# Kernel tuning notes

Hardware: AMD Instinct MI355X
Metric: run time of the kernel (lower is better)

Reference implementation:

```python
import jax, jax.numpy as jnp
import numpy as np

N = 50000  # nodes
NEG_SLOPE = 0.2


def gat_conv(x, src, dst, W, a_src, a_dst, b):
    # x: [N, in]; src/dst: [E'] (self-loops already appended)
    h = x @ W                                   # [N, out]
    alpha_s = h @ a_src                         # [N]
    alpha_d = h @ a_dst                         # [N]
    e = alpha_s[src] + alpha_d[dst]             # [E']
    e = jnp.where(e > 0, e, NEG_SLOPE * e)      # leaky_relu
    # segment softmax over destination neighborhoods
    m = jax.ops.segment_max(e, dst, num_segments=N)
    ex = jnp.exp(e - m[dst])
    denom = jax.ops.segment_sum(ex, dst, num_segments=N)
    alpha = ex / denom[dst]                     # [E']
    out = jax.ops.segment_sum(h[src] * alpha[:, None], dst, num_segments=N)
    return out + b


def setup_inputs() -> dict:
    key = jax.random.key(0)
    ks = jax.random.split(key, 16)
    d_in, d_hid, n_cls, E = 256, 256, 32, 400000
    inp = {
        "x": jax.random.normal(ks[0], (N, d_in), jnp.float32),
        "edge_index": jax.random.randint(ks[1], (2, E), 0, N, jnp.int64),
    }
    def glorot(k, shape):
        fan_in, fan_out = shape[0], shape[-1]
        s = jnp.sqrt(6.0 / (fan_in + fan_out))
        return jax.random.uniform(k, shape, jnp.float32, -s, s)
    inp["W0"] = glorot(ks[2], (d_in, d_hid)); inp["as0"] = glorot(ks[3], (1, d_hid))[0]; inp["ad0"] = glorot(ks[4], (1, d_hid))[0]; inp["b0"] = jnp.zeros((d_hid,), jnp.float32)
    inp["W1"] = glorot(ks[5], (d_hid, d_hid)); inp["as1"] = glorot(ks[6], (1, d_hid))[0]; inp["ad1"] = glorot(ks[7], (1, d_hid))[0]; inp["b1"] = jnp.zeros((d_hid,), jnp.float32)
    inp["W2"] = glorot(ks[8], (d_hid, n_cls)); inp["as2"] = glorot(ks[9], (1, n_cls))[0]; inp["ad2"] = glorot(ks[10], (1, n_cls))[0]; inp["b2"] = jnp.zeros((n_cls,), jnp.float32)
    return inp


def reference(x, edge_index, W0, as0, ad0, b0, W1, as1, ad1, b1, W2, as2, ad2, b2):
    # add self-loops (PyG GATConv default)
    loop = jnp.arange(N, dtype=edge_index.dtype)
    src = jnp.concatenate([edge_index[0], loop])
    dst = jnp.concatenate([edge_index[1], loop])
    h = x
    for (W, a_s, a_d, b) in [(W0, as0, ad0, b0), (W1, as1, ad1, b1)]:
        h = gat_conv(h, src, dst, W, a_s, a_d, b)
        h = h * jax.nn.sigmoid(h)  # swish gating
    h = gat_conv(h, src, dst, W2, as2, ad2, b2)
    return jax.nn.log_softmax(h, axis=1)
```

## Files before the change

### kernel.cpp

```cpp
#include <hip/hip_runtime.h>
#include <math.h>

#define N_NODES 50000
#define PAD_ROWS 50176
#define DUAL_BLOCKS 196
#define HALF_OFF (196 * 128)
#define E_RAW   400000
#define E_TOT   (E_RAW + N_NODES)
#define NEG_SLOPE 0.2f

typedef __bf16 bf16_t;
typedef bf16_t bf16x8 __attribute__((ext_vector_type(8)));
typedef bf16_t bf16x4 __attribute__((ext_vector_type(4)));
typedef float  f32x4  __attribute__((ext_vector_type(4)));

__device__ __forceinline__ void gll16(const void* g, void* l) {
    __builtin_amdgcn_global_load_lds(
        (const __attribute__((address_space(1))) void*)g,
        (__attribute__((address_space(3))) void*)l, 16, 0, 0);
}


__global__ void k_hist(const int* __restrict__ ei, int* __restrict__ cnt) {
    int e = blockIdx.x * 256 + threadIdx.x;
    if (e >= E_TOT) return;
    int dst = (e < E_RAW) ? ei[E_RAW + e] : (e - E_RAW);
    atomicAdd(&cnt[dst], 1);
}

__global__ void k_scan1(const int* __restrict__ cnt, int* __restrict__ offs,
                        int* __restrict__ bsum) {
    __shared__ int s[256];
    int i = blockIdx.x * 256 + threadIdx.x;
    int v = (i < N_NODES) ? cnt[i] : 0;
    s[threadIdx.x] = v;
    __syncthreads();
    for (int d = 1; d < 256; d <<= 1) {
        int t = (threadIdx.x >= d) ? s[threadIdx.x - d] : 0;
        __syncthreads();
        s[threadIdx.x] += t;
        __syncthreads();
    }
    if (i < N_NODES) offs[i] = s[threadIdx.x] - v;
    if (threadIdx.x == 255) bsum[blockIdx.x] = s[255];
}

__global__ void k_scan2(int* __restrict__ bsum, int nb) {
    __shared__ int s[256];
    int v = (threadIdx.x < nb) ? bsum[threadIdx.x] : 0;
    s[threadIdx.x] = v;
    __syncthreads();
    for (int d = 1; d < 256; d <<= 1) {
        int t = (threadIdx.x >= d) ? s[threadIdx.x - d] : 0;
        __syncthreads();
        s[threadIdx.x] += t;
        __syncthreads();
    }
    if (threadIdx.x < nb) bsum[threadIdx.x] = s[threadIdx.x] - v;
}

__global__ void k_scan3(int* __restrict__ offs, const int* __restrict__ bsum) {
    int i = blockIdx.x * 256 + threadIdx.x;
    if (i < N_NODES) offs[i] += bsum[blockIdx.x];
}

__global__ void k_scatter(const int* __restrict__ ei, const int* __restrict__ offs,
                          int* __restrict__ cursor, int* __restrict__ srcs,
                          int2* __restrict__ meta) {
    int e = blockIdx.x * 256 + threadIdx.x;
    if (e < 4) meta[E_TOT + e] = make_int2(0, 0);
    if (e >= E_TOT) return;
    int src, dst;
    if (e < E_RAW) { src = ei[e]; dst = ei[E_RAW + e]; }
    else           { src = dst = e - E_RAW; }
    int pos = offs[dst] + atomicAdd(&cursor[dst], 1);
    srcs[pos] = src;
}


__global__ void k_split_all(const float* __restrict__ W0, const float* __restrict__ W1,
                            const float* __restrict__ W2,
                            bf16_t* __restrict__ T0h, bf16_t* __restrict__ T0l,
                            bf16_t* __restrict__ T1h, bf16_t* __restrict__ T1l,
                            bf16_t* __restrict__ T2h, bf16_t* __restrict__ T2l,
                            int* __restrict__ cnts, int* __restrict__ cursor) {
    int idx = blockIdx.x * 256 + threadIdx.x;
    if (idx < N_NODES) { cnts[idx] = 0; cursor[idx] = 0; }
    float v; bf16_t *ph, *pl; int o;
    if (idx < 65536) {
        int k = idx >> 8, n = idx & 255;
        v = W0[idx]; ph = T0h; pl = T0l; o = n * 256 + k;
    } else if (idx < 131072) {
        int i = idx - 65536;
        int k = i >> 8, n = i & 255;
        v = W1[i]; ph = T1h; pl = T1l; o = n * 256 + k;
    } else if (idx < 139264) {
        int i = idx - 131072;
        int k = i >> 5, n = i & 31;
        v = W2[i]; ph = T2h; pl = T2l; o = n * 256 + k;
    } else return;
    bf16_t h = (bf16_t)v;
    ph[o] = h;
    pl[o] = (bf16_t)(v - (float)h);
}


template<bool A_FP32>
__global__ __launch_bounds__(512) void k_gemm256_dual(
        const float* __restrict__ Af, const bf16_t* __restrict__ Ab,
        const bf16_t* __restrict__ Bth,
        const float* __restrict__ a_s, const float* __restrict__ a_d,
        bf16_t* __restrict__ Hb, float* __restrict__ As, float* __restrict__ Ad) {
    __shared__ __align__(16) bf16_t Bs[16][8][512];

    const int tid  = threadIdx.x;
    const int lane = tid & 63;
    const int w    = tid >> 6;
    const int r16  = lane & 15;
    const int kg   = lane >> 4;

    #pragma unroll
    for (int i = 0; i < 16; ++i) {
        int op   = w * 16 + i;
        int nsub = op >> 3;
        int kk   = op & 7;
        gll16(&Bth[(nsub * 16 + r16) * 256 + kk * 32 + kg * 8], &Bs[nsub][kk][0]);
    }

    const int row0  = blockIdx.x * 128 + w * 16 + r16;
    const int row1  = row0 + HALF_OFF;
    const int rowc0 = min(row0, N_NODES - 1);
    const int rowc1 = min(row1, N_NODES - 1);
    const bool ok0  = row0 < N_NODES;
    const bool ok1  = row1 < N_NODES;

    bf16x8 x0[8], x1[8];
    if constexpr (A_FP32) {
        const float* a0 = Af + rowc0 * 256 + kg * 8;
        const float* a1 = Af + rowc1 * 256 + kg * 8;
        #pragma unroll
        for (int kk = 0; kk < 8; ++kk) {
            float4 v0 = *(const float4*)(a0 + kk * 32);
            float4 v1 = *(const float4*)(a0 + kk * 32 + 4);
            float4 u0 = *(const float4*)(a1 + kk * 32);
            float4 u1 = *(const float4*)(a1 + kk * 32 + 4);
            x0[kk] = bf16x8{(bf16_t)v0.x, (bf16_t)v0.y, (bf16_t)v0.z, (bf16_t)v0.w,
                            (bf16_t)v1.x, (bf16_t)v1.y, (bf16_t)v1.z, (bf16_t)v1.w};
            x1[kk] = bf16x8{(bf16_t)u0.x, (bf16_t)u0.y, (bf16_t)u0.z, (bf16_t)u0.w,
                            (bf16_t)u1.x, (bf16_t)u1.y, (bf16_t)u1.z, (bf16_t)u1.w};
        }
    } else {
        const bf16_t* a0 = Ab + rowc0 * 256 + kg * 8;
        const bf16_t* a1 = Ab + rowc1 * 256 + kg * 8;
        #pragma unroll
        for (int kk = 0; kk < 8; ++kk) {
            x0[kk] = *(const bf16x8*)(a0 + kk * 32);
            x1[kk] = *(const bf16x8*)(a1 + kk * 32);
        }
    }
    __syncthreads();

    f32x4 acc0[16] = {}, acc1[16] = {};
    #pragma unroll
    for (int kk = 0; kk < 8; ++kk) {
        #pragma unroll
        for (int n = 0; n < 16; ++n) {
            bf16x8 wf = *(const bf16x8*)&Bs[n][kk][lane * 8];
            acc0[n] = __builtin_amdgcn_mfma_f32_16x16x32_bf16(wf, x0[kk], acc0[n], 0, 0, 0);
            acc1[n] = __builtin_amdgcn_mfma_f32_16x16x32_bf16(wf, x1[kk], acc1[n], 0, 0, 0);
        }
    }

    {
        float ss = 0.f, sd = 0.f;
        #pragma unroll
        for (int n = 0; n < 16; ++n) {
            f32x4 v = acc0[n];
            if (ok0) {
                bf16x4 st = {(bf16_t)v[0], (bf16_t)v[1], (bf16_t)v[2], (bf16_t)v[3]};
                *(bf16x4*)&Hb[row0 * 256 + n * 16 + kg * 4] = st;
            }
            float4 a4 = *(const float4*)&a_s[n * 16 + kg * 4];
            float4 d4 = *(const float4*)&a_d[n * 16 + kg * 4];
            ss += v[0] * a4.x + v[1] * a4.y + v[2] * a4.z + v[3] * a4.w;
            sd += v[0] * d4.x + v[1] * d4.y + v[2] * d4.z + v[3] * d4.w;
        }
        ss += __shfl_xor(ss, 16); ss += __shfl_xor(ss, 32);
        sd += __shfl_xor(sd, 16); sd += __shfl_xor(sd, 32);
        if (ok0 && kg == 0) { As[row0] = ss; Ad[row0] = sd; }
    }
    {
        float ss = 0.f, sd = 0.f;
        #pragma unroll
        for (int n = 0; n < 16; ++n) {
            f32x4 v = acc1[n];
            if (ok1) {
                bf16x4 st = {(bf16_t)v[0], (bf16_t)v[1], (bf16_t)v[2], (bf16_t)v[3]};
                *(bf16x4*)&Hb[row1 * 256 + n * 16 + kg * 4] = st;
            }
            float4 a4 = *(const float4*)&a_s[n * 16 + kg * 4];
            float4 d4 = *(const float4*)&a_d[n * 16 + kg * 4];
            ss += v[0] * a4.x + v[1] * a4.y + v[2] * a4.z + v[3] * a4.w;
            sd += v[0] * d4.x + v[1] * d4.y + v[2] * d4.z + v[3] * d4.w;
        }
        ss += __shfl_xor(ss, 16); ss += __shfl_xor(ss, 32);
        sd += __shfl_xor(sd, 16); sd += __shfl_xor(sd, 32);
        if (ok1 && kg == 0) { As[row1] = ss; Ad[row1] = sd; }
    }
}


__global__ __launch_bounds__(512) void k_gemm256_cs(
        const bf16_t* __restrict__ Ab, const bf16_t* __restrict__ Bth,
        const float* __restrict__ a_s, const float* __restrict__ a_d,
        bf16_t* __restrict__ Hb,
        float* __restrict__ As0, float* __restrict__ Ad0,
        float* __restrict__ As1, float* __restrict__ Ad1) {
    __shared__ __align__(16) bf16_t Bs[8][8][512];

    const int pair = blockIdx.x >> 1;
    const int ch   = blockIdx.x & 1;
    const int tid  = threadIdx.x;
    const int lane = tid & 63;
    const int w    = tid >> 6;
    const int r16  = lane & 15;
    const int kg   = lane >> 4;
    const int cbase = ch * 128;

    #pragma unroll
    for (int i = 0; i < 8; ++i) {
        int op   = w * 8 + i;
        int nsub = op >> 3;
        int kk   = op & 7;
        gll16(&Bth[(cbase + nsub * 16 + r16) * 256 + kk * 32 + kg * 8], &Bs[nsub][kk][0]);
    }

    const int row0  = pair * 128 + w * 16 + r16;
    const int row1  = row0 + HALF_OFF;
    const int rowc0 = min(row0, N_NODES - 1);
    const int rowc1 = min(row1, N_NODES - 1);
    const bool ok0  = row0 < N_NODES;
    const bool ok1  = row1 < N_NODES;

    bf16x8 x0[8], x1[8];
    {
        const bf16_t* a0 = Ab + rowc0 * 256 + kg * 8;
        const bf16_t* a1 = Ab + rowc1 * 256 + kg * 8;
        #pragma unroll
        for (int kk = 0; kk < 8; ++kk) {
            x0[kk] = *(const bf16x8*)(a0 + kk * 32);
            x1[kk] = *(const bf16x8*)(a1 + kk * 32);
        }
    }
    __syncthreads();

    f32x4 acc0[8] = {}, acc1[8] = {};
    #pragma unroll
    for (int kk = 0; kk < 8; ++kk) {
        #pragma unroll
        for (int n = 0; n < 8; ++n) {
            bf16x8 wf = *(const bf16x8*)&Bs[n][kk][lane * 8];
            acc0[n] = __builtin_amdgcn_mfma_f32_16x16x32_bf16(wf, x0[kk], acc0[n], 0, 0, 0);
            acc1[n] = __builtin_amdgcn_mfma_f32_16x16x32_bf16(wf, x1[kk], acc1[n], 0, 0, 0);
        }
    }

    float* Asp = ch ? As1 : As0;
    float* Adp = ch ? Ad1 : Ad0;
    {
        float ss = 0.f, sd = 0.f;
        #pragma unroll
        for (int n = 0; n < 8; ++n) {
            f32x4 v = acc0[n];
            if (ok0) {
                bf16x4 st = {(bf16_t)v[0], (bf16_t)v[1], (bf16_t)v[2], (bf16_t)v[3]};
                *(bf16x4*)&Hb[row0 * 256 + cbase + n * 16 + kg * 4] = st;
            }
            float4 a4 = *(const float4*)&a_s[cbase + n * 16 + kg * 4];
            float4 d4 = *(const float4*)&a_d[cbase + n * 16 + kg * 4];
            ss += v[0] * a4.x + v[1] * a4.y + v[2] * a4.z + v[3] * a4.w;
            sd += v[0] * d4.x + v[1] * d4.y + v[2] * d4.z + v[3] * d4.w;
        }
        ss += __shfl_xor(ss, 16); ss += __shfl_xor(ss, 32);
        sd += __shfl_xor(sd, 16); sd += __shfl_xor(sd, 32);
        if (ok0 && kg == 0) { Asp[row0] = ss; Adp[row0] = sd; }
    }
    {
        float ss = 0.f, sd = 0.f;
        #pragma unroll
        for (int n = 0; n < 8; ++n) {
            f32x4 v = acc1[n];
            if (ok1) {
                bf16x4 st = {(bf16_t)v[0], (bf16_t)v[1], (bf16_t)v[2], (bf16_t)v[3]};
                *(bf16x4*)&Hb[row1 * 256 + cbase + n * 16 + kg * 4] = st;
            }
            float4 a4 = *(const float4*)&a_s[cbase + n * 16 + kg * 4];
            float4 d4 = *(const float4*)&a_d[cbase + n * 16 + kg * 4];
            ss += v[0] * a4.x + v[1] * a4.y + v[2] * a4.z + v[3] * a4.w;
            sd += v[0] * d4.x + v[1] * d4.y + v[2] * d4.z + v[3] * d4.w;
        }
        ss += __shfl_xor(ss, 16); ss += __shfl_xor(ss, 32);
        sd += __shfl_xor(sd, 16); sd += __shfl_xor(sd, 32);
        if (ok1 && kg == 0) { Asp[row1] = ss; Adp[row1] = sd; }
    }
}


__global__ __launch_bounds__(256) void k_gemm32_mfma(
        const bf16_t* __restrict__ Ab,
        const bf16_t* __restrict__ Bth, const bf16_t* __restrict__ Btl,
        const float* __restrict__ a_s, const float* __restrict__ a_d,
        float* __restrict__ Hc, float* __restrict__ As, float* __restrict__ Ad) {
    const int tid  = threadIdx.x;
    const int lane = tid & 63;
    const int wv   = tid >> 6;
    const int r16  = lane & 15;
    const int kg   = lane >> 4;
    const int rowg = blockIdx.x * 256 + wv * 64;

    int aoff[4], boff[2];
    #pragma unroll
    for (int m = 0; m < 4; ++m) {
        int row = rowg + m * 16 + r16;
        if (row >= N_NODES) row = N_NODES - 1;
        aoff[m] = row * 256 + kg * 8;
    }
    #pragma unroll
    for (int n = 0; n < 2; ++n)
        boff[n] = (n * 16 + r16) * 256 + kg * 8;

    f32x4 accT[2][4] = {};

    #pragma unroll
    for (int kk = 0; kk < 8; ++kk) {
        const int k0 = kk * 32;
        bf16x8 ah[4], bh[2], bl[2];
        #pragma unroll
        for (int m = 0; m < 4; ++m)
            ah[m] = *(const bf16x8*)(Ab + aoff[m] + k0);
        #pragma unroll
        for (int n = 0; n < 2; ++n) {
            bh[n] = *(const bf16x8*)(Bth + boff[n] + k0);
            bl[n] = *(const bf16x8*)(Btl + boff[n] + k0);
        }
        #pragma unroll
        for (int n = 0; n < 2; ++n) {
            #pragma unroll
            for (int m = 0; m < 4; ++m) {
                accT[n][m] = __builtin_amdgcn_mfma_f32_16x16x32_bf16(bh[n], ah[m], accT[n][m], 0, 0, 0);
                accT[n][m] = __builtin_amdgcn_mfma_f32_16x16x32_bf16(bl[n], ah[m], accT[n][m], 0, 0, 0);
            }
        }
    }

    float4 as4[2], ad4[2];
    #pragma unroll
    for (int n = 0; n < 2; ++n) {
        as4[n] = *(const float4*)&a_s[n * 16 + kg * 4];
        ad4[n] = *(const float4*)&a_d[n * 16 + kg * 4];
    }
    #pragma unroll
    for (int m = 0; m < 4; ++m) {
        int row = rowg + m * 16 + r16;
        bool ok = row < N_NODES;
        float ss = 0.f, sd = 0.f;
        #pragma unroll
        for (int n = 0; n < 2; ++n) {
            f32x4 v = accT[n][m];
            if (ok) {
                float4 st = {v[0], v[1], v[2], v[3]};
                *(float4*)&Hc[row * 32 + n * 16 + kg * 4] = st;
            }
            ss += v[0] * as4[n].x + v[1] * as4[n].y + v[2] * as4[n].z + v[3] * as4[n].w;
            sd += v[0] * ad4[n].x + v[1] * ad4[n].y + v[2] * ad4[n].z + v[3] * ad4[n].w;
        }
        ss += __shfl_xor(ss, 16); ss += __shfl_xor(ss, 32);
        sd += __shfl_xor(sd, 16); sd += __shfl_xor(sd, 32);
        if (ok && kg == 0) { As[row] = ss; Ad[row] = sd; }
    }
}


__global__ __launch_bounds__(256) void k_attn(
        const float* __restrict__ As0, const float* __restrict__ Ad0,
        const float* __restrict__ As1, const float* __restrict__ Ad1,
        const int dual,
        const int* __restrict__ offs, const int* __restrict__ cnts,
        const int* __restrict__ srcs,
        int2* __restrict__ meta, float* __restrict__ inv) {
    const int lane  = threadIdx.x & 63;
    const int wv    = threadIdx.x >> 6;
    const int g     = lane >> 3;
    const int gl    = lane & 7;
    const int node  = (blockIdx.x * 4 + wv) * 8 + g;
    if (node >= N_NODES) return;
    const int start = offs[node];
    const int cnt   = cnts[node];
    float ad = Ad0[node];
    if (dual) ad += Ad1[node];

    float m = -1e30f;
    for (int i = gl; i < cnt; i += 8) {
        int s = srcs[start + i];
        float as = As0[s];
        if (dual) as += As1[s];
        float e = as + ad;
        e = e > 0.f ? e : NEG_SLOPE * e;
        m = fmaxf(m, e);
    }
    m = fmaxf(m, __shfl_xor(m, 1));
    m = fmaxf(m, __shfl_xor(m, 2));
    m = fmaxf(m, __shfl_xor(m, 4));

    float denom = 0.f;
    for (int i = gl; i < cnt; i += 8) {
        int s = srcs[start + i];
        float as = As0[s];
        if (dual) as += As1[s];
        float e = as + ad;
        e = e > 0.f ? e : NEG_SLOPE * e;
        float p = __expf(e - m);
        denom += p;
        meta[start + i] = make_int2(s, __float_as_int(p));
    }
    denom += __shfl_xor(denom, 1);
    denom += __shfl_xor(denom, 2);
    denom += __shfl_xor(denom, 4);
    if (gl == 0) inv[node] = 1.f / denom;
}


__global__ __launch_bounds__(256) void k_gather256(
        const bf16_t* __restrict__ Hb, const int2* __restrict__ meta,
        const int* __restrict__ offs, const int* __restrict__ cnts,
        const float* __restrict__ inv,
        const float* __restrict__ bias, bf16_t* __restrict__ Hout) {
    const int gl   = threadIdx.x & 31;
    const int node = blockIdx.x * 8 + (threadIdx.x >> 5);
    if (node >= N_NODES) return;
    const int start = offs[node];
    const int cnt   = cnts[node];
    const float iv  = inv[node];
    const int c0 = gl * 8;

    float acc[8] = {};
    for (int j = 0; j < cnt; j += 4) {
        int2 mp[4];
        #pragma unroll
        for (int k = 0; k < 4; ++k) mp[k] = meta[start + j + k];
        #pragma unroll
        for (int k = 0; k < 4; ++k) {
            float p = (j + k < cnt) ? __int_as_float(mp[k].y) : 0.f;
            bf16x8 hv = *(const bf16x8*)&Hb[mp[k].x * 256 + c0];
            #pragma unroll
            for (int q = 0; q < 8; ++q) acc[q] += p * (float)hv[q];
        }
    }

    float4 b0 = *(const float4*)&bias[c0];
    float4 b1 = *(const float4*)&bias[c0 + 4];
    float bb[8] = {b0.x, b0.y, b0.z, b0.w, b1.x, b1.y, b1.z, b1.w};
    bf16x8 st;
    #pragma unroll
    for (int q = 0; q < 8; ++q) {
        float v = acc[q] * iv + bb[q];
        v = v / (1.f + __expf(-v));
        st[q] = (bf16_t)v;
    }
    *(bf16x8*)&Hout[node * 256 + c0] = st;
}


__global__ __launch_bounds__(256) void k_gather_final(
        const float* __restrict__ Hc,
        const int2* __restrict__ meta,
        const int* __restrict__ offs, const int* __restrict__ cnts,
        const float* __restrict__ inv,
        const float* __restrict__ bias, float* __restrict__ out) {
    const int gl   = threadIdx.x & 31;
    const int node = blockIdx.x * 8 + (threadIdx.x >> 5);
    if (node >= N_NODES) return;
    const int start = offs[node];
    const int cnt   = cnts[node];
    const float iv  = inv[node];

    float acc = 0.f;
    for (int j = 0; j < cnt; j += 4) {
        int2 mp[4];
        #pragma unroll
        for (int k = 0; k < 4; ++k) mp[k] = meta[start + j + k];
        #pragma unroll
        for (int k = 0; k < 4; ++k) {
            float p = (j + k < cnt) ? __int_as_float(mp[k].y) : 0.f;
            acc += p * Hc[mp[k].x * 32 + gl];
        }
    }

    float v = acc * iv + bias[gl];
    float mm = v;
    #pragma unroll
    for (int o = 16; o; o >>= 1) mm = fmaxf(mm, __shfl_xor(mm, o));
    float ex = __expf(v - mm), sum = ex;
    #pragma unroll
    for (int o = 16; o; o >>= 1) sum += __shfl_xor(sum, o);
    out[node * 32 + gl] = v - mm - __logf(sum);
}


extern "C" void kernel_launch(void* const* d_in, const int* in_sizes, int n_in,
                              void* d_out, int out_size, void* d_ws, size_t ws_size,
                              hipStream_t stream) {
    const float* x   = (const float*)d_in[0];
    const int*   ei  = (const int*)  d_in[1];
    const float* W0  = (const float*)d_in[2];
    const float* as0 = (const float*)d_in[3];
    const float* ad0 = (const float*)d_in[4];
    const float* b0  = (const float*)d_in[5];
    const float* W1  = (const float*)d_in[6];
    const float* as1 = (const float*)d_in[7];
    const float* ad1 = (const float*)d_in[8];
    const float* b1  = (const float*)d_in[9];
    const float* W2  = (const float*)d_in[10];
    const float* as2 = (const float*)d_in[11];
    const float* ad2 = (const float*)d_in[12];
    const float* b2  = (const float*)d_in[13];
    float* out = (float*)d_out;

    char* ws = (char*)d_ws;
    bf16_t* hA_b  = (bf16_t*)(ws + 0);
    bf16_t* hB_b  = (bf16_t*)(ws + 25690112);
    float*  hC    = (float*) (ws + 51380224);
    float*  As    = (float*) (ws + 57780224);
    float*  Ad    = (float*) (ws + 57980224);
    float*  inv   = (float*) (ws + 58180224);
    int*    cnts  = (int*)   (ws + 58380224);
    int*    cursor= (int*)   (ws + 58580224);
    int*    offs  = (int*)   (ws + 58780224);
    int*    srcs  = (int*)   (ws + 58980224);
    int2*   meta  = (int2*)  (ws + 60780224);
    int*    bsum  = (int*)   (ws + 64380288);
    bf16_t* Wth0  = (bf16_t*)(ws + 64381312);
    bf16_t* Wtl0  = (bf16_t*)(ws + 64512384);
    bf16_t* Wth1  = (bf16_t*)(ws + 64643456);
    bf16_t* Wtl1  = (bf16_t*)(ws + 64774528);
    bf16_t* Wth2  = (bf16_t*)(ws + 64905600);
    bf16_t* Wtl2  = (bf16_t*)(ws + 64921984);
    float*  As1p  = (float*) (ws + 64938368);
    float*  Ad1p  = (float*) (ws + 65138368);

    const int NB = (N_NODES + 255) / 256;

    k_split_all<<<544, 256, 0, stream>>>(W0, W1, W2, Wth0, Wtl0, Wth1, Wtl1,
                                         Wth2, Wtl2, cnts, cursor);
    k_hist   <<<(E_TOT + 255) / 256, 256, 0, stream>>>(ei, cnts);
    k_scan1  <<<NB, 256, 0, stream>>>(cnts, offs, bsum);
    k_scan2  <<<1, 256, 0, stream>>>(bsum, NB);
    k_scan3  <<<NB, 256, 0, stream>>>(offs, bsum);
    k_scatter<<<(E_TOT + 255) / 256, 256, 0, stream>>>(ei, offs, cursor, srcs, meta);

    const int GATHER_BLOCKS = (N_NODES + 7) / 8;
    const int ATTN_BLOCKS   = (N_NODES + 31) / 32;

    k_gemm256_dual<true><<<DUAL_BLOCKS, 512, 0, stream>>>(x, nullptr, Wth0, as0, ad0, hA_b, As, Ad);
    k_attn<<<ATTN_BLOCKS, 256, 0, stream>>>(As, Ad, As, Ad, 0, offs, cnts, srcs, meta, inv);
    k_gather256<<<GATHER_BLOCKS, 256, 0, stream>>>(hA_b, meta, offs, cnts, inv, b0, hB_b);
    k_gemm256_cs<<<DUAL_BLOCKS * 2, 512, 0, stream>>>(hB_b, Wth1, as1, ad1, hA_b, As, Ad, As1p, Ad1p);
    k_attn<<<ATTN_BLOCKS, 256, 0, stream>>>(As, Ad, As1p, Ad1p, 1, offs, cnts, srcs, meta, inv);
    k_gather256<<<GATHER_BLOCKS, 256, 0, stream>>>(hA_b, meta, offs, cnts, inv, b1, hB_b);
    k_gemm32_mfma<<<NB, 256, 0, stream>>>(hB_b, Wth2, Wtl2, as2, ad2, hC, As, Ad);
    k_attn<<<ATTN_BLOCKS, 256, 0, stream>>>(As, Ad, As, Ad, 0, offs, cnts, srcs, meta, inv);
    k_gather_final<<<GATHER_BLOCKS, 256, 0, stream>>>(hC, meta, offs, cnts, inv, b2, out);
}
```

Measured before the change: 236.6 us.

## Fuse attention softmax into gather kernels and merge scan passes

Removes the separate attention kernels that wrote per-edge (src, weight) metadata and an inverse denominator. Each gather now recomputes the leaky-relu score, exponentiates it without max subtraction and accumulates the denominator inline. This drops three launches and the per-edge metadata round trip through memory. It also merges the second and third scan kernels into one by having every block redo the small block-sum scan. The risk is overflow in exp without max stabilisation, plus redundant score computation in all 32 lanes per node.

Result: faster. 231.0 us (-2.4%).

```diff
diff --git a/kernel.cpp b/kernel.cpp
--- a/kernel.cpp
+++ b/kernel.cpp
@@ -45,7 +45,8 @@
     if (threadIdx.x == 255) bsum[blockIdx.x] = s[255];
 }
 
-__global__ void k_scan2(int* __restrict__ bsum, int nb) {
+__global__ void k_scan23(int* __restrict__ offs, const int* __restrict__ bsum,
+                         int nb) {
     __shared__ int s[256];
     int v = (threadIdx.x < nb) ? bsum[threadIdx.x] : 0;
     s[threadIdx.x] = v;
@@ -56,19 +57,15 @@
         s[threadIdx.x] += t;
         __syncthreads();
     }
-    if (threadIdx.x < nb) bsum[threadIdx.x] = s[threadIdx.x] - v;
-}
-
-__global__ void k_scan3(int* __restrict__ offs, const int* __restrict__ bsum) {
+    int add = (blockIdx.x == 0) ? 0 : s[blockIdx.x - 1];
     int i = blockIdx.x * 256 + threadIdx.x;
-    if (i < N_NODES) offs[i] += bsum[blockIdx.x];
+    if (i < N_NODES) offs[i] += add;
 }
 
 __global__ void k_scatter(const int* __restrict__ ei, const int* __restrict__ offs,
-                          int* __restrict__ cursor, int* __restrict__ srcs,
-                          int2* __restrict__ meta) {
+                          int* __restrict__ cursor, int* __restrict__ srcs) {
     int e = blockIdx.x * 256 + threadIdx.x;
-    if (e < 4) meta[E_TOT + e] = make_int2(0, 0);
+    if (e < 4) srcs[E_TOT + e] = 0;
     if (e >= E_TOT) return;
     int src, dst;
     if (e < E_RAW) { src = ei[e]; dst = ei[E_RAW + e]; }
@@ -381,81 +378,44 @@
 }
 
 
-__global__ __launch_bounds__(256) void k_attn(
+__global__ __launch_bounds__(256) void k_gather256_f(
+        const bf16_t* __restrict__ Hb,
         const float* __restrict__ As0, const float* __restrict__ Ad0,
         const float* __restrict__ As1, const float* __restrict__ Ad1,
         const int dual,
         const int* __restrict__ offs, const int* __restrict__ cnts,
         const int* __restrict__ srcs,
-        int2* __restrict__ meta, float* __restrict__ inv) {
-    const int lane  = threadIdx.x & 63;
-    const int wv    = threadIdx.x >> 6;
-    const int g     = lane >> 3;
-    const int gl    = lane & 7;
-    const int node  = (blockIdx.x * 4 + wv) * 8 + g;
-    if (node >= N_NODES) return;
-    const int start = offs[node];
-    const int cnt   = cnts[node];
-    float ad = Ad0[node];
-    if (dual) ad += Ad1[node];
-
-    float m = -1e30f;
-    for (int i = gl; i < cnt; i += 8) {
-        int s = srcs[start + i];
-        float as = As0[s];
-        if (dual) as += As1[s];
-        float e = as + ad;
-        e = e > 0.f ? e : NEG_SLOPE * e;
-        m = fmaxf(m, e);
-    }
-    m = fmaxf(m, __shfl_xor(m, 1));
-    m = fmaxf(m, __shfl_xor(m, 2));
-    m = fmaxf(m, __shfl_xor(m, 4));
-
-    float denom = 0.f;
-    for (int i = gl; i < cnt; i += 8) {
-        int s = srcs[start + i];
-        float as = As0[s];
-        if (dual) as += As1[s];
-        float e = as + ad;
-        e = e > 0.f ? e : NEG_SLOPE * e;
-        float p = __expf(e - m);
-        denom += p;
-        meta[start + i] = make_int2(s, __float_as_int(p));
-    }
-    denom += __shfl_xor(denom, 1);
-    denom += __shfl_xor(denom, 2);
-    denom += __shfl_xor(denom, 4);
-    if (gl == 0) inv[node] = 1.f / denom;
-}
-
-
-__global__ __launch_bounds__(256) void k_gather256(
-        const bf16_t* __restrict__ Hb, const int2* __restrict__ meta,
-        const int* __restrict__ offs, const int* __restrict__ cnts,
-        const float* __restrict__ inv,
         const float* __restrict__ bias, bf16_t* __restrict__ Hout) {
     const int gl   = threadIdx.x & 31;
     const int node = blockIdx.x * 8 + (threadIdx.x >> 5);
     if (node >= N_NODES) return;
     const int start = offs[node];
     const int cnt   = cnts[node];
-    const float iv  = inv[node];
+    float ad = Ad0[node];
+    if (dual) ad += Ad1[node];
     const int c0 = gl * 8;
 
     float acc[8] = {};
+    float denom = 0.f;
     for (int j = 0; j < cnt; j += 4) {
-        int2 mp[4];
-        #pragma unroll
-        for (int k = 0; k < 4; ++k) mp[k] = meta[start + j + k];
+        int s4[4];
+        #pragma unroll
+        for (int k = 0; k < 4; ++k) s4[k] = srcs[start + j + k];
         #pragma unroll
         for (int k = 0; k < 4; ++k) {
-            float p = (j + k < cnt) ? __int_as_float(mp[k].y) : 0.f;
-            bf16x8 hv = *(const bf16x8*)&Hb[mp[k].x * 256 + c0];
+            int s = s4[k];
+            float as = As0[s];
+            if (dual) as += As1[s];
+            float e = as + ad;
+            e = e > 0.f ? e : NEG_SLOPE * e;
+            float p = (j + k < cnt) ? __expf(e) : 0.f;
+            denom += p;
+            bf16x8 hv = *(const bf16x8*)&Hb[s * 256 + c0];
             #pragma unroll
             for (int q = 0; q < 8; ++q) acc[q] += p * (float)hv[q];
         }
     }
+    const float iv = 1.f / denom;
 
     float4 b0 = *(const float4*)&bias[c0];
     float4 b1 = *(const float4*)&bias[c0 + 4];
@@ -471,32 +431,36 @@
 }
 
 
-__global__ __launch_bounds__(256) void k_gather_final(
+__global__ __launch_bounds__(256) void k_gather_final_f(
         const float* __restrict__ Hc,
-        const int2* __restrict__ meta,
+        const float* __restrict__ As0, const float* __restrict__ Ad0,
         const int* __restrict__ offs, const int* __restrict__ cnts,
-        const float* __restrict__ inv,
+        const int* __restrict__ srcs,
         const float* __restrict__ bias, float* __restrict__ out) {
     const int gl   = threadIdx.x & 31;
     const int node = blockIdx.x * 8 + (threadIdx.x >> 5);
     if (node >= N_NODES) return;
     const int start = offs[node];
     const int cnt   = cnts[node];
-    const float iv  = inv[node];
-
-    float acc = 0.f;
+    const float ad  = Ad0[node];
+
+    float acc = 0.f, denom = 0.f;
     for (int j = 0; j < cnt; j += 4) {
-        int2 mp[4];
-        #pragma unroll
-        for (int k = 0; k < 4; ++k) mp[k] = meta[start + j + k];
+        int s4[4];
+        #pragma unroll
+        for (int k = 0; k < 4; ++k) s4[k] = srcs[start + j + k];
         #pragma unroll
         for (int k = 0; k < 4; ++k) {
-            float p = (j + k < cnt) ? __int_as_float(mp[k].y) : 0.f;
-            acc += p * Hc[mp[k].x * 32 + gl];
-        }
-    }
-
-    float v = acc * iv + bias[gl];
+            int s = s4[k];
+            float e = As0[s] + ad;
+            e = e > 0.f ? e : NEG_SLOPE * e;
+            float p = (j + k < cnt) ? __expf(e) : 0.f;
+            denom += p;
+            acc += p * Hc[s * 32 + gl];
+        }
+    }
+
+    float v = acc / denom + bias[gl];
     float mm = v;
     #pragma unroll
     for (int o = 16; o; o >>= 1) mm = fmaxf(mm, __shfl_xor(mm, o));
@@ -532,21 +496,19 @@
     float*  hC    = (float*) (ws + 51380224);
     float*  As    = (float*) (ws + 57780224);
     float*  Ad    = (float*) (ws + 57980224);
-    float*  inv   = (float*) (ws + 58180224);
     int*    cnts  = (int*)   (ws + 58380224);
     int*    cursor= (int*)   (ws + 58580224);
     int*    offs  = (int*)   (ws + 58780224);
     int*    srcs  = (int*)   (ws + 58980224);
-    int2*   meta  = (int2*)  (ws + 60780224);
-    int*    bsum  = (int*)   (ws + 64380288);
-    bf16_t* Wth0  = (bf16_t*)(ws + 64381312);
-    bf16_t* Wtl0  = (bf16_t*)(ws + 64512384);
-    bf16_t* Wth1  = (bf16_t*)(ws + 64643456);
-    bf16_t* Wtl1  = (bf16_t*)(ws + 64774528);
-    bf16_t* Wth2  = (bf16_t*)(ws + 64905600);
-    bf16_t* Wtl2  = (bf16_t*)(ws + 64921984);
-    float*  As1p  = (float*) (ws + 64938368);
-    float*  Ad1p  = (float*) (ws + 65138368);
+    int*    bsum  = (int*)   (ws + 60780240);
+    bf16_t* Wth0  = (bf16_t*)(ws + 60781264 + 48);
+    bf16_t* Wtl0  = (bf16_t*)(ws + 60912384);
+    bf16_t* Wth1  = (bf16_t*)(ws + 61043456);
+    bf16_t* Wtl1  = (bf16_t*)(ws + 61174528);
+    bf16_t* Wth2  = (bf16_t*)(ws + 61305600);
+    bf16_t* Wtl2  = (bf16_t*)(ws + 61321984);
+    float*  As1p  = (float*) (ws + 61338368);
+    float*  Ad1p  = (float*) (ws + 61538368);
 
     const int NB = (N_NODES + 255) / 256;
 
@@ -554,20 +516,15 @@
                                          Wth2, Wtl2, cnts, cursor);
     k_hist   <<<(E_TOT + 255) / 256, 256, 0, stream>>>(ei, cnts);
     k_scan1  <<<NB, 256, 0, stream>>>(cnts, offs, bsum);
-    k_scan2  <<<1, 256, 0, stream>>>(bsum, NB);
-    k_scan3  <<<NB, 256, 0, stream>>>(offs, bsum);
-    k_scatter<<<(E_TOT + 255) / 256, 256, 0, stream>>>(ei, offs, cursor, srcs, meta);
+    k_scan23 <<<NB, 256, 0, stream>>>(offs, bsum, NB);
+    k_scatter<<<(E_TOT + 255) / 256, 256, 0, stream>>>(ei, offs, cursor, srcs);
 
     const int GATHER_BLOCKS = (N_NODES + 7) / 8;
-    const int ATTN_BLOCKS   = (N_NODES + 31) / 32;
 
     k_gemm256_dual<true><<<DUAL_BLOCKS, 512, 0, stream>>>(x, nullptr, Wth0, as0, ad0, hA_b, As, Ad);
-    k_attn<<<ATTN_BLOCKS, 256, 0, stream>>>(As, Ad, As, Ad, 0, offs, cnts, srcs, meta, inv);
-    k_gather256<<<GATHER_BLOCKS, 256, 0, stream>>>(hA_b, meta, offs, cnts, inv, b0, hB_b);
+    k_gather256_f<<<GATHER_BLOCKS, 256, 0, stream>>>(hA_b, As, Ad, As, Ad, 0, offs, cnts, srcs, b0, hB_b);
     k_gemm256_cs<<<DUAL_BLOCKS * 2, 512, 0, stream>>>(hB_b, Wth1, as1, ad1, hA_b, As, Ad, As1p, Ad1p);
-    k_attn<<<ATTN_BLOCKS, 256, 0, stream>>>(As, Ad, As1p, Ad1p, 1, offs, cnts, srcs, meta, inv);
-    k_gather256<<<GATHER_BLOCKS, 256, 0, stream>>>(hA_b, meta, offs, cnts, inv, b1, hB_b);
+    k_gather256_f<<<GATHER_BLOCKS, 256, 0, stream>>>(hA_b, As, Ad, As1p, Ad1p, 1, offs, cnts, srcs, b1, hB_b);
     k_gemm32_mfma<<<NB, 256, 0, stream>>>(hB_b, Wth2, Wtl2, as2, ad2, hC, As, Ad);
-    k_attn<<<ATTN_BLOCKS, 256, 0, stream>>>(As, Ad, As, Ad, 0, offs, cnts, srcs, meta, inv);
-    k_gather_final<<<GATHER_BLOCKS, 256, 0, stream>>>(hC, meta, offs, cnts, inv, b2, out);
-}
+    k_gather_final_f<<<GATHER_BLOCKS, 256, 0, stream>>>(hC, As, Ad, offs, cnts, srcs, b2, out);
+}
```
